# Performance work log

Measured on AMD Instinct MI355X. Metric: run time of the kernel, lower is better.

The kernel has to match this reference:

```python
import jax, jax.numpy as jnp
import numpy as np

# ---- static config (from init_kwargs / search_cfg) ----
N, C, CI, H, W_ = 4, 64, 16, 96, 96   # frames, in_ch, inter_ch, height, width
PS, S0, WS, K = 7, 4, 9, 32           # patch size, query stride, search window, top-k
SCALE = 10.0                          # softmax_scale
WH, PP = WS // 2, PS // 2
PAD = WH + PP                         # reflect pad so every candidate patch is valid
nH = H // S0
NQ = nH * nH                          # queries per frame
D = CI * PS * PS                      # patch feature dim


def conv1x1(x, w, b):
    # x: [N,Cin,H,W], w: [Cout,Cin]
    return jnp.einsum('oc,nchw->nohw', w, x) + b[None, :, None, None]


def extract_patches(x):
    # x: [N,CI,H,W] -> [N,Ho,Wo,CI*PS*PS]; patch at index y has center y-WH in image coords
    xp = jnp.pad(x, ((0, 0), (0, 0), (PAD, PAD), (PAD, PAD)), mode='reflect')
    p = jax.lax.conv_general_dilated_patches(xp, (PS, PS), (1, 1), 'VALID')
    return jnp.transpose(p, (0, 2, 3, 1))


def setup_inputs() -> dict:
    key = jax.random.key(0)
    ks = jax.random.split(key, 6)
    s = 0.05
    return {
        'vid': jax.random.normal(ks[0], (N, C, H, W_), jnp.float32),
        'flows': jnp.zeros((N, 2, H, W_), jnp.int32),
        'theta_w': jax.random.normal(ks[1], (CI, C), jnp.float32) * s,
        'theta_b': jnp.zeros((CI,), jnp.float32),
        'phi_w': jax.random.normal(ks[2], (CI, C), jnp.float32) * s,
        'phi_b': jnp.zeros((CI,), jnp.float32),
        'g_w': jax.random.normal(ks[3], (CI, C), jnp.float32) * s,
        'g_b': jnp.zeros((CI,), jnp.float32),
        'w_w': jax.random.normal(ks[4], (C, CI), jnp.float32) * s,
        'w_b': jnp.zeros((C,), jnp.float32),
    }


def reference(vid, flows, theta_w, theta_b, phi_w, phi_b, g_w, g_b, w_w, w_b):
    theta = conv1x1(vid, theta_w, theta_b)   # queries
    phi = conv1x1(vid, phi_w, phi_b)         # keys
    g = conv1x1(vid, g_w, g_b)               # values

    Tp = extract_patches(theta)  # [N,Ho,Wo,D]
    Pp = extract_patches(phi)
    Gp = extract_patches(g)

    # query grid centers (stride0)
    q = jnp.arange(0, H, S0)
    qci = jnp.repeat(q, nH)      # [NQ]
    qcj = jnp.tile(q, nH)

    # flow-guided candidate window (stride1=1, ws x ws offsets)
    off = jnp.arange(WS) - WH
    oi = jnp.repeat(off, WS)     # [WS*WS]
    oj = jnp.tile(off, WS)
    fq = flows[:, :, qci, qcj]   # [N,2,NQ] integer flow at query centers
    ci = jnp.clip(qci[None, :, None] + fq[:, 0, :, None] + oi[None, None, :], 0, H - 1)
    cj = jnp.clip(qcj[None, :, None] + fq[:, 1, :, None] + oj[None, None, :], 0, W_ - 1)
    Yi, Yj = ci + WH, cj + WH    # [N,NQ,WS*WS] indices into patch arrays

    gather = jax.vmap(lambda P, yi, yj: P[yi, yj])

    Qp = Tp[:, qci + WH, qcj + WH, :]            # [N,NQ,D]
    Cg = gather(Pp, Yi, Yj)                      # [N,NQ,WS*WS,D]
    # L2 patch distances
    dist = ((Qp ** 2).sum(-1)[:, :, None] + (Cg ** 2).sum(-1)
            - 2.0 * jnp.einsum('nqd,nqwd->nqw', Qp, Cg))

    negd, idx = jax.lax.top_k(-dist, K)          # k nearest patches
    w = jax.nn.softmax(SCALE * negd, axis=-1)    # softmax(-scale * dist)

    yi_k = jnp.take_along_axis(Yi, idx, axis=2)  # [N,NQ,K]
    yj_k = jnp.take_along_axis(Yj, idx, axis=2)
    Gg = gather(Gp, yi_k, yj_k)                  # [N,NQ,K,D]

    # wpsum: weighted patch sum
    outp = jnp.einsum('nqk,nqkd->nqd', w, Gg).reshape(N, NQ, CI, PS, PS)
    vals = jnp.transpose(outp, (0, 1, 3, 4, 2))  # [N,NQ,PS,PS,CI]

    # fold (overlap-add) back to image, normalized by counts
    ii2 = (qci[:, None] + jnp.arange(PS))[:, :, None]   # [NQ,PS,1] canvas rows
    jj2 = (qcj[:, None] + jnp.arange(PS))[:, None, :]   # [NQ,1,PS] canvas cols
    Hc, Wc = H + 2 * PP, W_ + 2 * PP
    canvas = jnp.zeros((N, Hc, Wc, CI), vid.dtype).at[:, ii2, jj2, :].add(vals)
    cnt = jnp.zeros((Hc, Wc), vid.dtype).at[ii2, jj2].add(jnp.ones((NQ, PS, PS), vid.dtype))
    agg = canvas[:, PP:PP + H, PP:PP + W_] / cnt[PP:PP + H, PP:PP + W_, None]
    agg = jnp.transpose(agg, (0, 3, 1, 2))       # [N,CI,H,W]

    return vid + conv1x1(agg, w_w, w_b)
```

## Files before the change

### kernel.cpp

```cpp
#include <hip/hip_runtime.h>
#include <hip/hip_bf16.h>

#define N_   4
#define C_   64
#define CI_  16
#define H_   96
#define W__  96
#define PS_  7
#define S0_  4
#define WS_  9
#define K_   32
#define WH_  4
#define PP_  3
#define nH_  24
#define NQ_  576
#define D_   784
#define HW_  9216

#define PLS  226
#define QLS  52
#define GLS  16

__device__ __forceinline__ int rf(int v) {
    v = v < 0 ? -v : v;
    return v > H_ - 1 ? 2 * (H_ - 1) - v : v;
}

__global__ __launch_bounds__(256) void conv_kernel(
    const float* __restrict__ vid,
    const float* __restrict__ tw, const float* __restrict__ tb,
    const float* __restrict__ pw, const float* __restrict__ pb,
    const float* __restrict__ gw, const float* __restrict__ gb,
    float* __restrict__ theta, float* __restrict__ phi, float* __restrict__ g)
{
    int b = blockIdx.x;
    int pbk = b % 144;
    int t2  = b / 144;
    int og  = t2 & 1;
    int arr = t2 >> 1;
    const float* wsel = arr == 0 ? tw : (arr == 1 ? pw : gw);
    const float* bsel = arr == 0 ? tb : (arr == 1 ? pb : gb);
    float*       dsel = arr == 0 ? theta : (arr == 1 ? phi : g);

    int idx = pbk * 256 + threadIdx.x;
    int n = idx / HW_, pix = idx % HW_;
    const float* vp = vid + (size_t)n * C_ * HW_ + pix;
    const float* wp = wsel + og * 8 * C_;

    float v[64];
#pragma unroll
    for (int c = 0; c < 64; c++) v[c] = vp[c * HW_];

    float acc[8];
#pragma unroll
    for (int o = 0; o < 8; o++) acc[o] = 0.f;
#pragma unroll
    for (int o = 0; o < 8; o++) {
#pragma unroll
        for (int c = 0; c < 64; c += 4) {
            float4 w4 = *(const float4*)&wp[o * C_ + c];
            acc[o] += w4.x * v[c] + w4.y * v[c + 1] + w4.z * v[c + 2] + w4.w * v[c + 3];
        }
    }

    size_t ob = (size_t)idx * CI_ + og * 8;
    *(float4*)&dsel[ob + 0] = make_float4(acc[0] + bsel[og * 8 + 0],
                                          acc[1] + bsel[og * 8 + 1],
                                          acc[2] + bsel[og * 8 + 2],
                                          acc[3] + bsel[og * 8 + 3]);
    *(float4*)&dsel[ob + 4] = make_float4(acc[4] + bsel[og * 8 + 4],
                                          acc[5] + bsel[og * 8 + 5],
                                          acc[6] + bsel[og * 8 + 6],
                                          acc[7] + bsel[og * 8 + 7]);
}

__global__ __launch_bounds__(256) void attn_kernel(
    const float* __restrict__ theta, const float* __restrict__ phi,
    const float* __restrict__ g, const int* __restrict__ flows,
    float* __restrict__ outp)
{
    __shared__ float Ql[CI_ * QLS];
    __shared__ float Pl[CI_ * PLS];
    __shared__ __hip_bfloat16 Gl[225 * GLS];
    __shared__ float dist[81];
    __shared__ float distW[81];
    __shared__ float wlist[K_];
    __shared__ int   olist[K_];
    __shared__ float dmin_s;
    __shared__ int   cnt0_s;

    int tid = threadIdx.x;
    int bq  = blockIdx.x;
    int n = bq / NQ_, q0 = bq % NQ_;
    int qi = q0 / nH_, qj = q0 % nH_;
    int qci = qi * S0_, qcj = qj * S0_;

    int f0 = flows[((n * 2 + 0) * H_ + qci) * W__ + qcj];
    int f1 = flows[((n * 2 + 1) * H_ + qci) * W__ + qcj];
    int bi = qci + f0, bj = qcj + f1;
    int loi = min(max(bi - WH_, 0), H_ - 1);
    int loj = min(max(bj - WH_, 0), W__ - 1);

    const float* thn = theta + (size_t)n * HW_ * CI_;
    const float* phn = phi   + (size_t)n * HW_ * CI_;
    const float* gn  = g     + (size_t)n * HW_ * CI_;

    if (tid < 196) {
        int px = tid >> 2, cg = (tid & 3) * 4;
        int r = px / 7, s = px % 7;
        size_t gb = ((size_t)(rf(qci + r - PP_) * W__ + rf(qcj + s - PP_))) * CI_ + cg;
        float4 v = *(const float4*)&thn[gb];
        Ql[(cg + 0) * QLS + px] = v.x;
        Ql[(cg + 1) * QLS + px] = v.y;
        Ql[(cg + 2) * QLS + px] = v.z;
        Ql[(cg + 3) * QLS + px] = v.w;
    }
    for (int i = tid; i < 225 * 4; i += 256) {
        int px = i >> 2, cg = (i & 3) * 4;
        int r = px / 15, s = px % 15;
        size_t gb = ((size_t)(rf(loi + r - PP_) * W__ + rf(loj + s - PP_))) * CI_ + cg;
        float4 pv = *(const float4*)&phn[gb];
        float4 gv = *(const float4*)&gn[gb];
        Pl[(cg + 0) * PLS + px] = pv.x;
        Pl[(cg + 1) * PLS + px] = pv.y;
        Pl[(cg + 2) * PLS + px] = pv.z;
        Pl[(cg + 3) * PLS + px] = pv.w;
        Gl[px * GLS + cg + 0] = __float2bfloat16(gv.x);
        Gl[px * GLS + cg + 1] = __float2bfloat16(gv.y);
        Gl[px * GLS + cg + 2] = __float2bfloat16(gv.z);
        Gl[px * GLS + cg + 3] = __float2bfloat16(gv.w);
    }
    __syncthreads();

    if (tid < 144) {
        int c  = tid & 15;
        int cj = tid >> 4;
        float qr[49];
#pragma unroll
        for (int i2 = 0; i2 < 12; i2++) {
            float4 t4 = *(const float4*)&Ql[c * QLS + i2 * 4];
            qr[i2 * 4 + 0] = t4.x; qr[i2 * 4 + 1] = t4.y;
            qr[i2 * 4 + 2] = t4.z; qr[i2 * 4 + 3] = t4.w;
        }
        qr[48] = Ql[c * QLS + 48];

        float corr[9], sqv[9];
#pragma unroll
        for (int i2 = 0; i2 < 9; i2++) { corr[i2] = 0.f; sqv[i2] = 0.f; }

        const float* Pb = &Pl[c * PLS + cj];
#pragma unroll
        for (int y = 0; y < 15; y++) {
            float seg[7];
#pragma unroll
            for (int s = 0; s < 7; s++) seg[s] = Pb[y * 15 + s];
            float s2 = 0.f;
#pragma unroll
            for (int s = 0; s < 7; s++) s2 += seg[s] * seg[s];
#pragma unroll
            for (int ci = 0; ci < 9; ci++) {
                if (y - ci >= 0 && y - ci < 7) {
                    const int r = y - ci;
                    float t = 0.f;
#pragma unroll
                    for (int s = 0; s < 7; s++) t += qr[r * 7 + s] * seg[s];
                    corr[ci] += t;
                    sqv[ci]  += s2;
                }
            }
        }
#pragma unroll
        for (int ci = 0; ci < 9; ci++) {
            float v2 = sqv[ci] - 2.f * corr[ci];
#pragma unroll
            for (int m2 = 1; m2 < 16; m2 <<= 1) v2 += __shfl_xor(v2, m2, 16);
            if (c == ci) dist[cj * 9 + ci] = v2;
        }
    }
    __syncthreads();

    float d = 0.f;
    int cil = 0, cjl = 0;
    if (tid < 81) {
        int wi = tid / WS_, wj = tid % WS_;
        cil = min(max(bi + wi - WH_, 0), H_ - 1) - loi;
        cjl = min(max(bj + wj - WH_, 0), W__ - 1) - loj;
        d = dist[cjl * 9 + cil];
        distW[tid] = d;
    }
    __syncthreads();

    bool sel = false;
    if (tid < 81) {
        int rank = 0;
        for (int j = 0; j < 81; j++) {
            float dj = distW[j];
            rank += (dj < d) || (dj == d && j < tid);
        }
        sel = rank < K_;
        if (rank == 0) dmin_s = d;
    }
    unsigned long long m = __ballot(sel);
    if (tid == 0) cnt0_s = __popcll(m);
    __syncthreads();

    if (sel) {
        unsigned long long lt = ((unsigned long long)1 << (tid & 63)) - 1;
        int pos = __popcll(m & lt) + (tid >= 64 ? cnt0_s : 0);
        float e = expf(10.f * (dmin_s - d));
        wlist[pos] = e;
        olist[pos] = cil * 15 + cjl;
    }
    __syncthreads();

    float wreg[K_];
    int   oreg[K_];
    float esum = 0.f;
#pragma unroll
    for (int k = 0; k < K_; k++) {
        wreg[k] = wlist[k];
        esum += wreg[k];
        oreg[k] = olist[k] * GLS;
    }
    float inv_es = 1.f / esum;
#pragma unroll
    for (int k = 0; k < K_; k++) wreg[k] *= inv_es;

    float* op = outp + (size_t)bq * D_;
    for (int dI = tid; dI < D_; dI += 256) {
        int rs = dI >> 4, c = dI & 15;
        int r = rs / 7, s = rs % 7;
        int base2 = (r * 15 + s) * GLS + c;
        float acc = 0.f;
#pragma unroll
        for (int k = 0; k < K_; k++)
            acc += wreg[k] * __bfloat162float(Gl[oreg[k] + base2]);
        op[dI] = acc;
    }
}

__global__ __launch_bounds__(256) void output_kernel(
    const float* __restrict__ vid, const float* __restrict__ outp,
    const float* __restrict__ ww, const float* __restrict__ wb,
    float* __restrict__ out)
{
    int tid = threadIdx.x;
    int og  = blockIdx.y;
    int idx = blockIdx.x * 256 + tid;
    int n = idx / HW_, pix = idx % HW_;
    int y = pix / W__, x = pix % W__;
    int tlo_i = y >> 2, tlo_j = x >> 2;
    int thi_i = min(nH_ - 1, (y + PP_) >> 2);
    int thi_j = min(nH_ - 1, (x + PP_) >> 2);
    int ni = thi_i - tlo_i + 1;
    int nj = thi_j - tlo_j + 1;
    float inv = 1.f / (float)(ni * nj);

    float agg[CI_];
#pragma unroll
    for (int c = 0; c < CI_; c++) agg[c] = 0.f;

#pragma unroll
    for (int cb = 0; cb < 4; cb++) {
        int qi = tlo_i + (cb >> 1);
        int qj = tlo_j + (cb & 1);
        if (qi <= thi_i && qj <= thi_j) {
            int a  = y + PP_ - S0_ * qi;
            int bb = x + PP_ - S0_ * qj;
            const float* op = outp +
                (((size_t)n * NQ_ + qi * nH_ + qj) * 49 + a * 7 + bb) * CI_;
            float4 r0 = *(const float4*)&op[0];
            float4 r1 = *(const float4*)&op[4];
            float4 r2 = *(const float4*)&op[8];
            float4 r3 = *(const float4*)&op[12];
            agg[0] += r0.x; agg[1] += r0.y; agg[2]  += r0.z; agg[3]  += r0.w;
            agg[4] += r1.x; agg[5] += r1.y; agg[6]  += r1.z; agg[7]  += r1.w;
            agg[8] += r2.x; agg[9] += r2.y; agg[10] += r2.z; agg[11] += r2.w;
            agg[12] += r3.x; agg[13] += r3.y; agg[14] += r3.z; agg[15] += r3.w;
        }
    }
#pragma unroll
    for (int c = 0; c < CI_; c++) agg[c] *= inv;

    const float* vp  = vid + (size_t)n * C_ * HW_ + pix;
    float*       op2 = out + (size_t)n * C_ * HW_ + pix;
#pragma unroll
    for (int oo = 0; oo < 8; oo++) {
        int co = og * 8 + oo;
        float4 w0 = *(const float4*)&ww[co * CI_ + 0];
        float4 w1 = *(const float4*)&ww[co * CI_ + 4];
        float4 w2 = *(const float4*)&ww[co * CI_ + 8];
        float4 w3 = *(const float4*)&ww[co * CI_ + 12];
        float s = wb[co];
        s += w0.x * agg[0]  + w0.y * agg[1]  + w0.z * agg[2]  + w0.w * agg[3];
        s += w1.x * agg[4]  + w1.y * agg[5]  + w1.z * agg[6]  + w1.w * agg[7];
        s += w2.x * agg[8]  + w2.y * agg[9]  + w2.z * agg[10] + w2.w * agg[11];
        s += w3.x * agg[12] + w3.y * agg[13] + w3.z * agg[14] + w3.w * agg[15];
        op2[(size_t)co * HW_] = vp[(size_t)co * HW_] + s;
    }
}

extern "C" void kernel_launch(void* const* d_in, const int* in_sizes, int n_in,
                              void* d_out, int out_size, void* d_ws, size_t ws_size,
                              hipStream_t stream) {
    const float* vid   = (const float*)d_in[0];
    const int*   flows = (const int*)  d_in[1];
    const float* tw    = (const float*)d_in[2];
    const float* tb    = (const float*)d_in[3];
    const float* pw    = (const float*)d_in[4];
    const float* pb    = (const float*)d_in[5];
    const float* gw    = (const float*)d_in[6];
    const float* gb    = (const float*)d_in[7];
    const float* ww    = (const float*)d_in[8];
    const float* wb    = (const float*)d_in[9];
    float* out = (float*)d_out;

    float* ws = (float*)d_ws;
    const size_t fsz = (size_t)N_ * HW_ * CI_;
    float* theta = ws;
    float* phi   = ws + fsz;
    float* g     = ws + 2 * fsz;
    float* outp  = ws + 3 * fsz;

    conv_kernel<<<864, 256, 0, stream>>>(
        vid, tw, tb, pw, pb, gw, gb, theta, phi, g);
    attn_kernel<<<N_ * NQ_, 256, 0, stream>>>(theta, phi, g, flows, outp);
    output_kernel<<<dim3(144, 8), 256, 0, stream>>>(vid, outp, ww, wb, out);
}
```

Before: 132.7 us.

## Fuse three kernels into one cooperative persistent kernel with grid syncs

Replaces the conv, attention and output kernels with a single persistent kernel of 768 blocks. It runs each stage as a grid-stride loop separated by cooperative grid syncs, and falls back to three launches if the cooperative launch fails. The attention stage now handles three queries per block, stores phi in pixel-major layout, packs g as bf16 pairs, and computes four channels per thread in the weighted sum. This is meant to remove launch gaps and tail effects between stages, at the cost of grid-sync overhead and fewer, heavier blocks.

```diff
diff --git a/kernel.cpp b/kernel.cpp
--- a/kernel.cpp
+++ b/kernel.cpp
@@ -1,12 +1,14 @@
 #include <hip/hip_runtime.h>
 #include <hip/hip_bf16.h>
+#include <hip/hip_cooperative_groups.h>
+
+namespace cg = cooperative_groups;
 
 #define N_   4
 #define C_   64
 #define CI_  16
 #define H_   96
 #define W__  96
-#define PS_  7
 #define S0_  4
 #define WS_  9
 #define K_   32
@@ -16,287 +18,297 @@
 #define NQ_  576
 #define D_   784
 #define HW_  9216
-
-#define PLS  226
+#define NQT  2304
+#define GRID_ 768
 #define QLS  52
-#define GLS  16
+
+typedef unsigned int uint_t;
+typedef unsigned long long ull_t;
 
 __device__ __forceinline__ int rf(int v) {
     v = v < 0 ? -v : v;
     return v > H_ - 1 ? 2 * (H_ - 1) - v : v;
 }
 
-__global__ __launch_bounds__(256) void conv_kernel(
-    const float* __restrict__ vid,
+__device__ __forceinline__ uint_t bf16pair(float x, float y) {
+    uint_t ux = __float_as_uint(x), uy = __float_as_uint(y);
+    ux = (ux + 0x7fffu + ((ux >> 16) & 1u)) >> 16;
+    uy = (uy + 0x7fffu + ((uy >> 16) & 1u)) & 0xffff0000u;
+    return ux | uy;
+}
+
+__global__ __launch_bounds__(256, 3) void fused_kernel(
+    const float* __restrict__ vid, const int* __restrict__ flows,
     const float* __restrict__ tw, const float* __restrict__ tb,
     const float* __restrict__ pw, const float* __restrict__ pb,
     const float* __restrict__ gw, const float* __restrict__ gb,
-    float* __restrict__ theta, float* __restrict__ phi, float* __restrict__ g)
+    const float* __restrict__ ww, const float* __restrict__ wb,
+    float* __restrict__ theta, float* __restrict__ phi, float* __restrict__ gf,
+    float* __restrict__ outp, float* __restrict__ out,
+    int phase_mask, int coop)
 {
-    int b = blockIdx.x;
-    int pbk = b % 144;
-    int t2  = b / 144;
-    int og  = t2 & 1;
-    int arr = t2 >> 1;
-    const float* wsel = arr == 0 ? tw : (arr == 1 ? pw : gw);
-    const float* bsel = arr == 0 ? tb : (arr == 1 ? pb : gb);
-    float*       dsel = arr == 0 ? theta : (arr == 1 ? phi : g);
-
-    int idx = pbk * 256 + threadIdx.x;
-    int n = idx / HW_, pix = idx % HW_;
-    const float* vp = vid + (size_t)n * C_ * HW_ + pix;
-    const float* wp = wsel + og * 8 * C_;
-
-    float v[64];
-#pragma unroll
-    for (int c = 0; c < 64; c++) v[c] = vp[c * HW_];
-
-    float acc[8];
-#pragma unroll
-    for (int o = 0; o < 8; o++) acc[o] = 0.f;
-#pragma unroll
-    for (int o = 0; o < 8; o++) {
-#pragma unroll
-        for (int c = 0; c < 64; c += 4) {
-            float4 w4 = *(const float4*)&wp[o * C_ + c];
-            acc[o] += w4.x * v[c] + w4.y * v[c + 1] + w4.z * v[c + 2] + w4.w * v[c + 3];
+    cg::grid_group gg = cg::this_grid();
+    const int tid = threadIdx.x;
+    const int bid = blockIdx.x;
+
+    __shared__ float  Ql[CI_ * QLS];
+    __shared__ float  Pl[225 * CI_];
+    __shared__ uint_t Gu[225 * 8];
+    __shared__ float  dist[81];
+    __shared__ float  distW[81];
+    __shared__ float  wlist[K_];
+    __shared__ int    olist[K_];
+    __shared__ float  dmin_s;
+    __shared__ int    cnt0_s;
+
+    if (phase_mask & 1) {
+        for (int t = bid * 256 + tid; t < 6 * N_ * HW_; t += GRID_ * 256) {
+            int arr = __builtin_amdgcn_readfirstlane(t / (2 * N_ * HW_));
+            int og  = __builtin_amdgcn_readfirstlane((t / (N_ * HW_)) & 1);
+            int idx = t % (N_ * HW_);
+            const float* wsel = arr == 0 ? tw : (arr == 1 ? pw : gw);
+            const float* bsel = arr == 0 ? tb : (arr == 1 ? pb : gb);
+            float*       dsel = arr == 0 ? theta : (arr == 1 ? phi : gf);
+
+            int n = idx / HW_, pix = idx % HW_;
+            const float* vp = vid + (size_t)n * C_ * HW_ + pix;
+            const float* wp = wsel + og * 8 * C_;
+
+            float v[64];
+#pragma unroll
+            for (int c = 0; c < 64; c++) v[c] = vp[c * HW_];
+
+            float acc[8];
+#pragma unroll
+            for (int o = 0; o < 8; o++) acc[o] = 0.f;
+#pragma unroll
+            for (int o = 0; o < 8; o++) {
+#pragma unroll
+                for (int c = 0; c < 64; c += 4) {
+                    float4 w4 = *(const float4*)&wp[o * C_ + c];
+                    acc[o] += w4.x * v[c] + w4.y * v[c + 1]
+                            + w4.z * v[c + 2] + w4.w * v[c + 3];
+                }
+            }
+            size_t ob = (size_t)idx * CI_ + og * 8;
+            *(float4*)&dsel[ob + 0] = make_float4(acc[0] + bsel[og * 8 + 0],
+                                                  acc[1] + bsel[og * 8 + 1],
+                                                  acc[2] + bsel[og * 8 + 2],
+                                                  acc[3] + bsel[og * 8 + 3]);
+            *(float4*)&dsel[ob + 4] = make_float4(acc[4] + bsel[og * 8 + 4],
+                                                  acc[5] + bsel[og * 8 + 5],
+                                                  acc[6] + bsel[og * 8 + 6],
+                                                  acc[7] + bsel[og * 8 + 7]);
         }
     }
-
-    size_t ob = (size_t)idx * CI_ + og * 8;
-    *(float4*)&dsel[ob + 0] = make_float4(acc[0] + bsel[og * 8 + 0],
-                                          acc[1] + bsel[og * 8 + 1],
-                                          acc[2] + bsel[og * 8 + 2],
-                                          acc[3] + bsel[og * 8 + 3]);
-    *(float4*)&dsel[ob + 4] = make_float4(acc[4] + bsel[og * 8 + 4],
-                                          acc[5] + bsel[og * 8 + 5],
-                                          acc[6] + bsel[og * 8 + 6],
-                                          acc[7] + bsel[og * 8 + 7]);
-}
-
-__global__ __launch_bounds__(256) void attn_kernel(
-    const float* __restrict__ theta, const float* __restrict__ phi,
-    const float* __restrict__ g, const int* __restrict__ flows,
-    float* __restrict__ outp)
-{
-    __shared__ float Ql[CI_ * QLS];
-    __shared__ float Pl[CI_ * PLS];
-    __shared__ __hip_bfloat16 Gl[225 * GLS];
-    __shared__ float dist[81];
-    __shared__ float distW[81];
-    __shared__ float wlist[K_];
-    __shared__ int   olist[K_];
-    __shared__ float dmin_s;
-    __shared__ int   cnt0_s;
-
-    int tid = threadIdx.x;
-    int bq  = blockIdx.x;
-    int n = bq / NQ_, q0 = bq % NQ_;
-    int qi = q0 / nH_, qj = q0 % nH_;
-    int qci = qi * S0_, qcj = qj * S0_;
-
-    int f0 = flows[((n * 2 + 0) * H_ + qci) * W__ + qcj];
-    int f1 = flows[((n * 2 + 1) * H_ + qci) * W__ + qcj];
-    int bi = qci + f0, bj = qcj + f1;
-    int loi = min(max(bi - WH_, 0), H_ - 1);
-    int loj = min(max(bj - WH_, 0), W__ - 1);
-
-    const float* thn = theta + (size_t)n * HW_ * CI_;
-    const float* phn = phi   + (size_t)n * HW_ * CI_;
-    const float* gn  = g     + (size_t)n * HW_ * CI_;
-
-    if (tid < 196) {
-        int px = tid >> 2, cg = (tid & 3) * 4;
-        int r = px / 7, s = px % 7;
-        size_t gb = ((size_t)(rf(qci + r - PP_) * W__ + rf(qcj + s - PP_))) * CI_ + cg;
-        float4 v = *(const float4*)&thn[gb];
-        Ql[(cg + 0) * QLS + px] = v.x;
-        Ql[(cg + 1) * QLS + px] = v.y;
-        Ql[(cg + 2) * QLS + px] = v.z;
-        Ql[(cg + 3) * QLS + px] = v.w;
-    }
-    for (int i = tid; i < 225 * 4; i += 256) {
-        int px = i >> 2, cg = (i & 3) * 4;
-        int r = px / 15, s = px % 15;
-        size_t gb = ((size_t)(rf(loi + r - PP_) * W__ + rf(loj + s - PP_))) * CI_ + cg;
-        float4 pv = *(const float4*)&phn[gb];
-        float4 gv = *(const float4*)&gn[gb];
-        Pl[(cg + 0) * PLS + px] = pv.x;
-        Pl[(cg + 1) * PLS + px] = pv.y;
-        Pl[(cg + 2) * PLS + px] = pv.z;
-        Pl[(cg + 3) * PLS + px] = pv.w;
-        Gl[px * GLS + cg + 0] = __float2bfloat16(gv.x);
-        Gl[px * GLS + cg + 1] = __float2bfloat16(gv.y);
-        Gl[px * GLS + cg + 2] = __float2bfloat16(gv.z);
-        Gl[px * GLS + cg + 3] = __float2bfloat16(gv.w);
-    }
-    __syncthreads();
-
-    if (tid < 144) {
-        int c  = tid & 15;
-        int cj = tid >> 4;
-        float qr[49];
-#pragma unroll
-        for (int i2 = 0; i2 < 12; i2++) {
-            float4 t4 = *(const float4*)&Ql[c * QLS + i2 * 4];
-            qr[i2 * 4 + 0] = t4.x; qr[i2 * 4 + 1] = t4.y;
-            qr[i2 * 4 + 2] = t4.z; qr[i2 * 4 + 3] = t4.w;
-        }
-        qr[48] = Ql[c * QLS + 48];
-
-        float corr[9], sqv[9];
-#pragma unroll
-        for (int i2 = 0; i2 < 9; i2++) { corr[i2] = 0.f; sqv[i2] = 0.f; }
-
-        const float* Pb = &Pl[c * PLS + cj];
-#pragma unroll
-        for (int y = 0; y < 15; y++) {
-            float seg[7];
-#pragma unroll
-            for (int s = 0; s < 7; s++) seg[s] = Pb[y * 15 + s];
-            float s2 = 0.f;
-#pragma unroll
-            for (int s = 0; s < 7; s++) s2 += seg[s] * seg[s];
-#pragma unroll
-            for (int ci = 0; ci < 9; ci++) {
-                if (y - ci >= 0 && y - ci < 7) {
-                    const int r = y - ci;
-                    float t = 0.f;
-#pragma unroll
-                    for (int s = 0; s < 7; s++) t += qr[r * 7 + s] * seg[s];
-                    corr[ci] += t;
-                    sqv[ci]  += s2;
-                }
-            }
-        }
-#pragma unroll
-        for (int ci = 0; ci < 9; ci++) {
-            float v2 = sqv[ci] - 2.f * corr[ci];
-#pragma unroll
-            for (int m2 = 1; m2 < 16; m2 <<= 1) v2 += __shfl_xor(v2, m2, 16);
-            if (c == ci) dist[cj * 9 + ci] = v2;
+    if (coop) gg.sync();
+
+    if (phase_mask & 2) {
+        const int c3rs = tid >> 2;
+        const int c3cg = tid & 3;
+        const int rmapC3 = (c3rs / 7) * 15 + (c3rs % 7);
+
+        for (int it = 0; it < 3; it++) {
+            int bq = bid * 3 + it;
+            int n = bq / NQ_, q0 = bq % NQ_;
+            int qi = q0 / nH_, qj = q0 % nH_;
+            int qci = qi * S0_, qcj = qj * S0_;
+
+            int f0 = flows[((n * 2 + 0) * H_ + qci) * W__ + qcj];
+            int f1 = flows[((n * 2 + 1) * H_ + qci) * W__ + qcj];
+            int bi = qci + f0, bj = qcj + f1;
+            int loi = min(max(bi - WH_, 0), H_ - 1);
+            int loj = min(max(bj - WH_, 0), W__ - 1);
+
+            const float* thn = theta + (size_t)n * HW_ * CI_;
+            const float* phn = phi   + (size_t)n * HW_ * CI_;
+            const float* gn  = gf    + (size_t)n * HW_ * CI_;
+
+            if (tid < 196) {
+                int px = tid >> 2, cg = (tid & 3) * 4;
+                int r = px / 7, s = px % 7;
+                size_t gb = ((size_t)(rf(qci + r - PP_) * W__ + rf(qcj + s - PP_))) * CI_ + cg;
+                float4 v = *(const float4*)&thn[gb];
+                Ql[(cg + 0) * QLS + px] = v.x;
+                Ql[(cg + 1) * QLS + px] = v.y;
+                Ql[(cg + 2) * QLS + px] = v.z;
+                Ql[(cg + 3) * QLS + px] = v.w;
+            }
+            for (int i = tid; i < 225 * 4; i += 256) {
+                int px = i >> 2, cg = (i & 3) * 4;
+                int r = px / 15, s = px % 15;
+                size_t gb = ((size_t)(rf(loi + r - PP_) * W__ + rf(loj + s - PP_))) * CI_ + cg;
+                float4 pv = *(const float4*)&phn[gb];
+                float4 gv = *(const float4*)&gn[gb];
+                *(float4*)&Pl[px * CI_ + cg] = pv;
+                Gu[px * 8 + (cg >> 1) + 0] = bf16pair(gv.x, gv.y);
+                Gu[px * 8 + (cg >> 1) + 1] = bf16pair(gv.z, gv.w);
+            }
+            __syncthreads();
+
+            if (tid < 144) {
+                int c  = tid & 15;
+                int cj = tid >> 4;
+                float qr[49];
+#pragma unroll
+                for (int i2 = 0; i2 < 12; i2++) {
+                    float4 t4 = *(const float4*)&Ql[c * QLS + i2 * 4];
+                    qr[i2 * 4 + 0] = t4.x; qr[i2 * 4 + 1] = t4.y;
+                    qr[i2 * 4 + 2] = t4.z; qr[i2 * 4 + 3] = t4.w;
+                }
+                qr[48] = Ql[c * QLS + 48];
+
+                float corr[9], sqv[9];
+#pragma unroll
+                for (int i2 = 0; i2 < 9; i2++) { corr[i2] = 0.f; sqv[i2] = 0.f; }
+
+#pragma unroll
+                for (int y = 0; y < 15; y++) {
+                    float seg[7];
+#pragma unroll
+                    for (int s = 0; s < 7; s++) seg[s] = Pl[(y * 15 + cj + s) * CI_ + c];
+                    float s2 = 0.f;
+#pragma unroll
+                    for (int s = 0; s < 7; s++) s2 += seg[s] * seg[s];
+#pragma unroll
+                    for (int ci = 0; ci < 9; ci++) {
+                        if (y - ci >= 0 && y - ci < 7) {
+                            const int r = y - ci;
+                            float tacc = 0.f;
+#pragma unroll
+                            for (int s = 0; s < 7; s++) tacc += qr[r * 7 + s] * seg[s];
+                            corr[ci] += tacc;
+                            sqv[ci]  += s2;
+                        }
+                    }
+                }
+#pragma unroll
+                for (int ci = 0; ci < 9; ci++) {
+                    float v2 = sqv[ci] - 2.f * corr[ci];
+#pragma unroll
+                    for (int m2 = 1; m2 < 16; m2 <<= 1) v2 += __shfl_xor(v2, m2, 16);
+                    if (c == ci) dist[cj * 9 + ci] = v2;
+                }
+            }
+            __syncthreads();
+
+            float d = 0.f;
+            int cil = 0, cjl = 0;
+            if (tid < 81) {
+                int wi = tid / WS_, wj = tid % WS_;
+                cil = min(max(bi + wi - WH_, 0), H_ - 1) - loi;
+                cjl = min(max(bj + wj - WH_, 0), W__ - 1) - loj;
+                d = dist[cjl * 9 + cil];
+                distW[tid] = d;
+            }
+            __syncthreads();
+
+            bool sel = false;
+            if (tid < 81) {
+                int rank = 0;
+                for (int j = 0; j < 81; j++) {
+                    float dj = distW[j];
+                    rank += (dj < d) || (dj == d && j < tid);
+                }
+                sel = rank < K_;
+                if (rank == 0) dmin_s = d;
+            }
+            ull_t m = __ballot(sel);
+            if (tid == 0) cnt0_s = __popcll(m);
+            __syncthreads();
+
+            if (sel) {
+                ull_t lt = ((ull_t)1 << (tid & 63)) - 1;
+                int pos = __popcll(m & lt) + (tid >= 64 ? cnt0_s : 0);
+                wlist[pos] = expf(10.f * (dmin_s - d));
+                olist[pos] = cil * 15 + cjl;
+            }
+            __syncthreads();
+
+            if (tid < 196) {
+                float wreg[K_];
+                int   oreg[K_];
+                float esum = 0.f;
+#pragma unroll
+                for (int k = 0; k < K_; k++) {
+                    wreg[k] = wlist[k];
+                    esum += wreg[k];
+                    oreg[k] = olist[k];
+                }
+                float inv_es = 1.f / esum;
+                float a0 = 0.f, a1 = 0.f, a2 = 0.f, a3 = 0.f;
+#pragma unroll
+                for (int k = 0; k < K_; k++) {
+                    uint2 gv2 = *(const uint2*)&Gu[(oreg[k] + rmapC3) * 8 + c3cg * 2];
+                    float g0 = __uint_as_float(gv2.x << 16);
+                    float g1 = __uint_as_float(gv2.x & 0xffff0000u);
+                    float g2 = __uint_as_float(gv2.y << 16);
+                    float g3 = __uint_as_float(gv2.y & 0xffff0000u);
+                    float wk = wreg[k];
+                    a0 += wk * g0; a1 += wk * g1; a2 += wk * g2; a3 += wk * g3;
+                }
+                *(float4*)&outp[(size_t)bq * D_ + c3rs * 16 + c3cg * 4] =
+                    make_float4(a0 * inv_es, a1 * inv_es, a2 * inv_es, a3 * inv_es);
+            }
+            __syncthreads();
         }
     }
-    __syncthreads();
-
-    float d = 0.f;
-    int cil = 0, cjl = 0;
-    if (tid < 81) {
-        int wi = tid / WS_, wj = tid % WS_;
-        cil = min(max(bi + wi - WH_, 0), H_ - 1) - loi;
-        cjl = min(max(bj + wj - WH_, 0), W__ - 1) - loj;
-        d = dist[cjl * 9 + cil];
-        distW[tid] = d;
-    }
-    __syncthreads();
-
-    bool sel = false;
-    if (tid < 81) {
-        int rank = 0;
-        for (int j = 0; j < 81; j++) {
-            float dj = distW[j];
-            rank += (dj < d) || (dj == d && j < tid);
+    if (coop) gg.sync();
+
+    if (phase_mask & 4) {
+        for (int t = bid * 256 + tid; t < 8 * N_ * HW_; t += GRID_ * 256) {
+            int og  = __builtin_amdgcn_readfirstlane(t / (N_ * HW_));
+            int idx = t % (N_ * HW_);
+            int n = idx / HW_, pix = idx % HW_;
+            int y = pix / W__, x = pix % W__;
+            int tlo_i = y >> 2, tlo_j = x >> 2;
+            int thi_i = min(nH_ - 1, (y + PP_) >> 2);
+            int thi_j = min(nH_ - 1, (x + PP_) >> 2);
+            float inv = 1.f / (float)((thi_i - tlo_i + 1) * (thi_j - tlo_j + 1));
+
+            float agg[CI_];
+#pragma unroll
+            for (int c = 0; c < CI_; c++) agg[c] = 0.f;
+
+#pragma unroll
+            for (int cb = 0; cb < 4; cb++) {
+                int qi = tlo_i + (cb >> 1);
+                int qj = tlo_j + (cb & 1);
+                if (qi <= thi_i && qj <= thi_j) {
+                    int a  = y + PP_ - S0_ * qi;
+                    int bb = x + PP_ - S0_ * qj;
+                    const float* op = outp +
+                        (((size_t)n * NQ_ + qi * nH_ + qj) * 49 + a * 7 + bb) * CI_;
+                    float4 r0 = *(const float4*)&op[0];
+                    float4 r1 = *(const float4*)&op[4];
+                    float4 r2 = *(const float4*)&op[8];
+                    float4 r3 = *(const float4*)&op[12];
+                    agg[0] += r0.x; agg[1] += r0.y; agg[2]  += r0.z; agg[3]  += r0.w;
+                    agg[4] += r1.x; agg[5] += r1.y; agg[6]  += r1.z; agg[7]  += r1.w;
+                    agg[8] += r2.x; agg[9] += r2.y; agg[10] += r2.z; agg[11] += r2.w;
+                    agg[12] += r3.x; agg[13] += r3.y; agg[14] += r3.z; agg[15] += r3.w;
+                }
+            }
+#pragma unroll
+            for (int c = 0; c < CI_; c++) agg[c] *= inv;
+
+            const float* vp  = vid + (size_t)n * C_ * HW_ + pix;
+            float*       op2 = out + (size_t)n * C_ * HW_ + pix;
+#pragma unroll
+            for (int oo = 0; oo < 8; oo++) {
+                int co = og * 8 + oo;
+                float4 w0 = *(const float4*)&ww[co * CI_ + 0];
+                float4 w1 = *(const float4*)&ww[co * CI_ + 4];
+                float4 w2 = *(const float4*)&ww[co * CI_ + 8];
+                float4 w3 = *(const float4*)&ww[co * CI_ + 12];
+                float s = wb[co];
+                s += w0.x * agg[0]  + w0.y * agg[1]  + w0.z * agg[2]  + w0.w * agg[3];
+                s += w1.x * agg[4]  + w1.y * agg[5]  + w1.z * agg[6]  + w1.w * agg[7];
+                s += w2.x * agg[8]  + w2.y * agg[9]  + w2.z * agg[10] + w2.w * agg[11];
+                s += w3.x * agg[12] + w3.y * agg[13] + w3.z * agg[14] + w3.w * agg[15];
+                op2[(size_t)co * HW_] = vp[(size_t)co * HW_] + s;
+            }
         }
-        sel = rank < K_;
-        if (rank == 0) dmin_s = d;
-    }
-    unsigned long long m = __ballot(sel);
-    if (tid == 0) cnt0_s = __popcll(m);
-    __syncthreads();
-
-    if (sel) {
-        unsigned long long lt = ((unsigned long long)1 << (tid & 63)) - 1;
-        int pos = __popcll(m & lt) + (tid >= 64 ? cnt0_s : 0);
-        float e = expf(10.f * (dmin_s - d));
-        wlist[pos] = e;
-        olist[pos] = cil * 15 + cjl;
-    }
-    __syncthreads();
-
-    float wreg[K_];
-    int   oreg[K_];
-    float esum = 0.f;
-#pragma unroll
-    for (int k = 0; k < K_; k++) {
-        wreg[k] = wlist[k];
-        esum += wreg[k];
-        oreg[k] = olist[k] * GLS;
-    }
-    float inv_es = 1.f / esum;
-#pragma unroll
-    for (int k = 0; k < K_; k++) wreg[k] *= inv_es;
-
-    float* op = outp + (size_t)bq * D_;
-    for (int dI = tid; dI < D_; dI += 256) {
-        int rs = dI >> 4, c = dI & 15;
-        int r = rs / 7, s = rs % 7;
-        int base2 = (r * 15 + s) * GLS + c;
-        float acc = 0.f;
-#pragma unroll
-        for (int k = 0; k < K_; k++)
-            acc += wreg[k] * __bfloat162float(Gl[oreg[k] + base2]);
-        op[dI] = acc;
-    }
-}
-
-__global__ __launch_bounds__(256) void output_kernel(
-    const float* __restrict__ vid, const float* __restrict__ outp,
-    const float* __restrict__ ww, const float* __restrict__ wb,
-    float* __restrict__ out)
-{
-    int tid = threadIdx.x;
-    int og  = blockIdx.y;
-    int idx = blockIdx.x * 256 + tid;
-    int n = idx / HW_, pix = idx % HW_;
-    int y = pix / W__, x = pix % W__;
-    int tlo_i = y >> 2, tlo_j = x >> 2;
-    int thi_i = min(nH_ - 1, (y + PP_) >> 2);
-    int thi_j = min(nH_ - 1, (x + PP_) >> 2);
-    int ni = thi_i - tlo_i + 1;
-    int nj = thi_j - tlo_j + 1;
-    float inv = 1.f / (float)(ni * nj);
-
-    float agg[CI_];
-#pragma unroll
-    for (int c = 0; c < CI_; c++) agg[c] = 0.f;
-
-#pragma unroll
-    for (int cb = 0; cb < 4; cb++) {
-        int qi = tlo_i + (cb >> 1);
-        int qj = tlo_j + (cb & 1);
-        if (qi <= thi_i && qj <= thi_j) {
-            int a  = y + PP_ - S0_ * qi;
-            int bb = x + PP_ - S0_ * qj;
-            const float* op = outp +
-                (((size_t)n * NQ_ + qi * nH_ + qj) * 49 + a * 7 + bb) * CI_;
-            float4 r0 = *(const float4*)&op[0];
-            float4 r1 = *(const float4*)&op[4];
-            float4 r2 = *(const float4*)&op[8];
-            float4 r3 = *(const float4*)&op[12];
-            agg[0] += r0.x; agg[1] += r0.y; agg[2]  += r0.z; agg[3]  += r0.w;
-            agg[4] += r1.x; agg[5] += r1.y; agg[6]  += r1.z; agg[7]  += r1.w;
-            agg[8] += r2.x; agg[9] += r2.y; agg[10] += r2.z; agg[11] += r2.w;
-            agg[12] += r3.x; agg[13] += r3.y; agg[14] += r3.z; agg[15] += r3.w;
-        }
-    }
-#pragma unroll
-    for (int c = 0; c < CI_; c++) agg[c] *= inv;
-
-    const float* vp  = vid + (size_t)n * C_ * HW_ + pix;
-    float*       op2 = out + (size_t)n * C_ * HW_ + pix;
-#pragma unroll
-    for (int oo = 0; oo < 8; oo++) {
-        int co = og * 8 + oo;
-        float4 w0 = *(const float4*)&ww[co * CI_ + 0];
-        float4 w1 = *(const float4*)&ww[co * CI_ + 4];
-        float4 w2 = *(const float4*)&ww[co * CI_ + 8];
-        float4 w3 = *(const float4*)&ww[co * CI_ + 12];
-        float s = wb[co];
-        s += w0.x * agg[0]  + w0.y * agg[1]  + w0.z * agg[2]  + w0.w * agg[3];
-        s += w1.x * agg[4]  + w1.y * agg[5]  + w1.z * agg[6]  + w1.w * agg[7];
-        s += w2.x * agg[8]  + w2.y * agg[9]  + w2.z * agg[10] + w2.w * agg[11];
-        s += w3.x * agg[12] + w3.y * agg[13] + w3.z * agg[14] + w3.w * agg[15];
-        op2[(size_t)co * HW_] = vp[(size_t)co * HW_] + s;
     }
 }
 
@@ -322,8 +334,22 @@
     float* g     = ws + 2 * fsz;
     float* outp  = ws + 3 * fsz;
 
-    conv_kernel<<<864, 256, 0, stream>>>(
-        vid, tw, tb, pw, pb, gw, gb, theta, phi, g);
-    attn_kernel<<<N_ * NQ_, 256, 0, stream>>>(theta, phi, g, flows, outp);
-    output_kernel<<<dim3(144, 8), 256, 0, stream>>>(vid, outp, ww, wb, out);
+    int mask_all = 7, coop1 = 1;
+    void* args[] = {
+        (void*)&vid, (void*)&flows, (void*)&tw, (void*)&tb, (void*)&pw, (void*)&pb,
+        (void*)&gw, (void*)&gb, (void*)&ww, (void*)&wb,
+        (void*)&theta, (void*)&phi, (void*)&g, (void*)&outp, (void*)&out,
+        (void*)&mask_all, (void*)&coop1
+    };
+    hipError_t rc = hipLaunchCooperativeKernel((const void*)fused_kernel,
+                                               dim3(GRID_), dim3(256),
+                                               args, 0, stream);
+    if (rc != hipSuccess) {
+        fused_kernel<<<GRID_, 256, 0, stream>>>(vid, flows, tw, tb, pw, pb, gw, gb,
+                                                ww, wb, theta, phi, g, outp, out, 1, 0);
+        fused_kernel<<<GRID_, 256, 0, stream>>>(vid, flows, tw, tb, pw, pb, gw, gb,
+                                                ww, wb, theta, phi, g, outp, out, 2, 0);
+        fused_kernel<<<GRID_, 256, 0, stream>>>(vid, flows, tw, tb, pw, pb, gw, gb,
+                                                ww, wb, theta, phi, g, outp, out, 4, 0);
+    }
 }
```

Result: slower. 333.6 us (+151.3%).

## Read theta/phi/g directly from global memory instead of staging tiles in LDS

Applied to the files above, without the earlier changes.

The attention kernel no longer stages the query, key and value windows in shared memory. It precomputes reflected row/column offsets in small LDS tables and reads theta, phi and g straight from global memory (through cache) in the distance and weighted-sum loops. The weighted sum now uses float4 gathers in fp32 instead of bf16 LDS values. The block drops to 192 threads with a launch-bounds occupancy hint. This removes the LDS staging and the barrier it needed, but trades them for many scattered, partly uncoalesced global loads (per-channel strided reads for phi) that depend on cache hits.

```diff
diff --git a/kernel.cpp b/kernel.cpp
--- a/kernel.cpp
+++ b/kernel.cpp
@@ -17,10 +17,6 @@
 #define D_   784
 #define HW_  9216
 
-#define PLS  226
-#define QLS  52
-#define GLS  16
-
 __device__ __forceinline__ int rf(int v) {
     v = v < 0 ? -v : v;
     return v > H_ - 1 ? 2 * (H_ - 1) - v : v;
@@ -74,15 +70,15 @@
                                           acc[7] + bsel[og * 8 + 7]);
 }
 
-__global__ __launch_bounds__(256) void attn_kernel(
+__global__ __launch_bounds__(192, 4) void attn_kernel(
     const float* __restrict__ theta, const float* __restrict__ phi,
     const float* __restrict__ g, const int* __restrict__ flows,
     float* __restrict__ outp)
 {
-    __shared__ float Ql[CI_ * QLS];
-    __shared__ float Pl[CI_ * PLS];
-    __shared__ __hip_bfloat16 Gl[225 * GLS];
-    __shared__ float dist[81];
+    __shared__ int   rowL[15], colL[15];
+    __shared__ int   qrowL[7], qcolL[7];
+    __shared__ int   rcL[225];
+    __shared__ float dist_cc[81];
     __shared__ float distW[81];
     __shared__ float wlist[K_];
     __shared__ int   olist[K_];
@@ -105,55 +101,39 @@
     const float* phn = phi   + (size_t)n * HW_ * CI_;
     const float* gn  = g     + (size_t)n * HW_ * CI_;
 
-    if (tid < 196) {
-        int px = tid >> 2, cg = (tid & 3) * 4;
-        int r = px / 7, s = px % 7;
-        size_t gb = ((size_t)(rf(qci + r - PP_) * W__ + rf(qcj + s - PP_))) * CI_ + cg;
-        float4 v = *(const float4*)&thn[gb];
-        Ql[(cg + 0) * QLS + px] = v.x;
-        Ql[(cg + 1) * QLS + px] = v.y;
-        Ql[(cg + 2) * QLS + px] = v.z;
-        Ql[(cg + 3) * QLS + px] = v.w;
-    }
-    for (int i = tid; i < 225 * 4; i += 256) {
-        int px = i >> 2, cg = (i & 3) * 4;
-        int r = px / 15, s = px % 15;
-        size_t gb = ((size_t)(rf(loi + r - PP_) * W__ + rf(loj + s - PP_))) * CI_ + cg;
-        float4 pv = *(const float4*)&phn[gb];
-        float4 gv = *(const float4*)&gn[gb];
-        Pl[(cg + 0) * PLS + px] = pv.x;
-        Pl[(cg + 1) * PLS + px] = pv.y;
-        Pl[(cg + 2) * PLS + px] = pv.z;
-        Pl[(cg + 3) * PLS + px] = pv.w;
-        Gl[px * GLS + cg + 0] = __float2bfloat16(gv.x);
-        Gl[px * GLS + cg + 1] = __float2bfloat16(gv.y);
-        Gl[px * GLS + cg + 2] = __float2bfloat16(gv.z);
-        Gl[px * GLS + cg + 3] = __float2bfloat16(gv.w);
-    }
-    __syncthreads();
+    if (tid < 15) {
+        rowL[tid] = rf(loi + tid - PP_) * W__;
+        colL[tid] = rf(loj + tid - PP_);
+    }
+    if (tid >= 32 && tid < 39) {
+        int s = tid - 32;
+        qrowL[s] = rf(qci + s - PP_) * W__;
+        qcolL[s] = rf(qcj + s - PP_);
+    }
+    __syncthreads();
+    for (int i = tid; i < 225; i += 192) rcL[i] = rowL[i / 15] + colL[i % 15];
 
     if (tid < 144) {
         int c  = tid & 15;
         int cj = tid >> 4;
         float qr[49];
 #pragma unroll
-        for (int i2 = 0; i2 < 12; i2++) {
-            float4 t4 = *(const float4*)&Ql[c * QLS + i2 * 4];
-            qr[i2 * 4 + 0] = t4.x; qr[i2 * 4 + 1] = t4.y;
-            qr[i2 * 4 + 2] = t4.z; qr[i2 * 4 + 3] = t4.w;
-        }
-        qr[48] = Ql[c * QLS + 48];
+        for (int r = 0; r < 7; r++)
+#pragma unroll
+            for (int s = 0; s < 7; s++)
+                qr[r * 7 + s] = thn[(size_t)(qrowL[r] + qcolL[s]) * CI_ + c];
 
         float corr[9], sqv[9];
 #pragma unroll
         for (int i2 = 0; i2 < 9; i2++) { corr[i2] = 0.f; sqv[i2] = 0.f; }
 
-        const float* Pb = &Pl[c * PLS + cj];
 #pragma unroll
         for (int y = 0; y < 15; y++) {
+            int rv = rowL[y];
             float seg[7];
 #pragma unroll
-            for (int s = 0; s < 7; s++) seg[s] = Pb[y * 15 + s];
+            for (int s = 0; s < 7; s++)
+                seg[s] = phn[(size_t)(rv + colL[cj + s]) * CI_ + c];
             float s2 = 0.f;
 #pragma unroll
             for (int s = 0; s < 7; s++) s2 += seg[s] * seg[s];
@@ -174,7 +154,7 @@
             float v2 = sqv[ci] - 2.f * corr[ci];
 #pragma unroll
             for (int m2 = 1; m2 < 16; m2 <<= 1) v2 += __shfl_xor(v2, m2, 16);
-            if (c == ci) dist[cj * 9 + ci] = v2;
+            if (c == ci) dist_cc[cj * 9 + ci] = v2;
         }
     }
     __syncthreads();
@@ -185,7 +165,7 @@
         int wi = tid / WS_, wj = tid % WS_;
         cil = min(max(bi + wi - WH_, 0), H_ - 1) - loi;
         cjl = min(max(bj + wj - WH_, 0), W__ - 1) - loj;
-        d = dist[cjl * 9 + cil];
+        d = dist_cc[cjl * 9 + cil];
         distW[tid] = d;
     }
     __syncthreads();
@@ -207,9 +187,8 @@
     if (sel) {
         unsigned long long lt = ((unsigned long long)1 << (tid & 63)) - 1;
         int pos = __popcll(m & lt) + (tid >= 64 ? cnt0_s : 0);
-        float e = expf(10.f * (dmin_s - d));
-        wlist[pos] = e;
-        olist[pos] = cil * 15 + cjl;
+        wlist[pos] = expf(10.f * (dmin_s - d));
+        olist[pos] = (cil << 4) | cjl;
     }
     __syncthreads();
 
@@ -220,22 +199,26 @@
     for (int k = 0; k < K_; k++) {
         wreg[k] = wlist[k];
         esum += wreg[k];
-        oreg[k] = olist[k] * GLS;
+        oreg[k] = olist[k];
     }
     float inv_es = 1.f / esum;
 #pragma unroll
     for (int k = 0; k < K_; k++) wreg[k] *= inv_es;
 
     float* op = outp + (size_t)bq * D_;
-    for (int dI = tid; dI < D_; dI += 256) {
-        int rs = dI >> 4, c = dI & 15;
+    for (int t = tid; t < 196; t += 192) {
+        int rs = t >> 2, cg = (t & 3) * 4;
         int r = rs / 7, s = rs % 7;
-        int base2 = (r * 15 + s) * GLS + c;
-        float acc = 0.f;
-#pragma unroll
-        for (int k = 0; k < K_; k++)
-            acc += wreg[k] * __bfloat162float(Gl[oreg[k] + base2]);
-        op[dI] = acc;
+        float a0 = 0.f, a1 = 0.f, a2 = 0.f, a3 = 0.f;
+#pragma unroll
+        for (int k = 0; k < K_; k++) {
+            int o  = oreg[k];
+            int rc = rcL[((o >> 4) + r) * 15 + (o & 15) + s];
+            float4 gv = *(const float4*)&gn[(size_t)rc * CI_ + cg];
+            float wk = wreg[k];
+            a0 += wk * gv.x; a1 += wk * gv.y; a2 += wk * gv.z; a3 += wk * gv.w;
+        }
+        *(float4*)&op[rs * CI_ + cg] = make_float4(a0, a1, a2, a3);
     }
 }
 
@@ -324,6 +307,6 @@
 
     conv_kernel<<<864, 256, 0, stream>>>(
         vid, tw, tb, pw, pb, gw, gb, theta, phi, g);
-    attn_kernel<<<N_ * NQ_, 256, 0, stream>>>(theta, phi, g, flows, outp);
+    attn_kernel<<<N_ * NQ_, 192, 0, stream>>>(theta, phi, g, flows, outp);
     output_kernel<<<dim3(144, 8), 256, 0, stream>>>(vid, outp, ww, wb, out);
 }
```

Result: slower. 182.6 us (+37.6%).
